# Performance work log

Hardware: AMD Instinct MI355X
Metric: run time of the kernel (lower is better)

Reference implementation:

```python
import jax, jax.numpy as jnp
import numpy as np

B, T, CIN, F, K, U, FF, N, LS = 16, 384, 64, 64, 32, 128, 1024, 64, 15
EPS = 1e-3  # keras BatchNormalization epsilon

def _conv1d(x, w):
    # x:[B,T,C], w:[K,C,F], 'same' padding, no bias
    return jax.lax.conv_general_dilated(x, w, (1,), 'SAME', dimension_numbers=('NWC', 'WIO', 'NWC'))

def _bn(x, g, b, m, v):
    # inference-mode batchnorm
    return g * (x - m) * jax.lax.rsqrt(v + EPS) + b

def _gru_seq(x, k, rk, b):
    # keras GRU (reset_after=True), gate order [z, r, h]; x:[B,T,D] -> [B,T,U]
    u = rk.shape[0]
    xp = x @ k + b[0]                      # precompute input projections [B,T,3U]
    def step(h, xt):
        rec = h @ rk + b[1]
        xz, xr, xh = jnp.split(xt, 3, axis=-1)
        rz, rr_, rh = jnp.split(rec, 3, axis=-1)
        z = jax.nn.sigmoid(xz + rz)
        r = jax.nn.sigmoid(xr + rr_)
        hh = jnp.tanh(xh + r * rh)
        hn = z * h + (1.0 - z) * hh
        return hn, hn
    h0 = jnp.zeros((x.shape[0], u), x.dtype)
    _, ys = jax.lax.scan(step, h0, jnp.swapaxes(xp, 0, 1))
    return jnp.swapaxes(ys, 0, 1)

def _cgru(xr, xi, kr, rkr, br, ki, rki, bi):
    # ComplexGRUCell: real_gru applied to both parts, imag_gru applied to both parts
    rr = _gru_seq(xr, kr, rkr, br)
    ri = _gru_seq(xi, kr, rkr, br)
    ir = _gru_seq(xr, ki, rki, bi)
    ii = _gru_seq(xi, ki, rki, bi)
    return rr - ii, ri + ir

def _forward(h_real, h_imag, conv_wr, conv_wi, bn_gr, bn_br, bn_mr, bn_vr, bn_gi, bn_bi, bn_mi, bn_vi, g0_kr, g0_rkr, g0_br, g0_ki, g0_rki, g0_bi, gs_kr, gs_rkr, gs_br, gs_ki, gs_rki, gs_bi, ff1_w, ff1_b, ff2_w, ff2_b, qr_w, qr_b, qi_w, qi_b, rr_w, rr_b, ri_w, ri_b):
    xr = _bn(_conv1d(h_real, conv_wr) - _conv1d(h_imag, conv_wi), bn_gr, bn_br, bn_mr, bn_vr)
    xi = _bn(_conv1d(h_imag, conv_wr) + _conv1d(h_real, conv_wi), bn_gi, bn_bi, bn_mi, bn_vi)
    xr, xi = _cgru(xr, xi, g0_kr, g0_rkr, g0_br, g0_ki, g0_rki, g0_bi)
    for i in range(LS):  # fixed small layer count
        xr, xi = _cgru(xr, xi, gs_kr[i], gs_rkr[i], gs_br[i], gs_ki[i], gs_rki[i], gs_bi[i])
    def ff(a):
        return jax.nn.relu(a @ ff1_w + ff1_b) @ ff2_w + ff2_b
    xr = xr + ff(xr)   # dropout is identity at inference
    xi = xi + ff(xi)
    mr = jnp.mean(xr, axis=1)
    mi = jnp.mean(xi, axis=1)
    Qr = (mr @ qr_w + qr_b) - (mi @ qi_w + qi_b)
    Qi = (mi @ qr_w + qr_b) + (mr @ qi_w + qi_b)
    Rr = (mr @ rr_w + rr_b) - (mi @ ri_w + ri_b)
    Ri = (mi @ rr_w + rr_b) + (mr @ ri_w + ri_b)
    Qr = Qr.reshape(-1, N, N); Qi = Qi.reshape(-1, N, N)
    Rr = Rr.reshape(-1, N, N); Ri = Ri.reshape(-1, N, N)
    # trace(Q Q^H) = sum |Q|^2 (real, nonnegative)
    nrm = jnp.sqrt(jnp.sum(Qr * Qr + Qi * Qi, axis=(1, 2)))[:, None, None]
    scale = jnp.sqrt(jnp.float32(N)) / nrm
    return Qr * scale, Qi * scale, Rr, Ri

def setup_inputs():
    key = jax.random.key(0)
    ks = jax.random.split(key, 20)
    s = 0.05
    def nrm(k, shape, scale=s):
        return jax.random.normal(k, shape, jnp.float32) * scale
    inp = {}
    inp['h_real'] = nrm(ks[0], (B, T, CIN), 1.0)
    inp['h_imag'] = nrm(ks[1], (B, T, CIN), 1.0)
    inp['conv_wr'] = nrm(ks[2], (K, CIN, F))
    inp['conv_wi'] = nrm(ks[3], (K, CIN, F))
    for nm in ('bn_gr', 'bn_gi', 'bn_vr', 'bn_vi'):
        inp[nm] = jnp.ones((F,), jnp.float32)
    for nm in ('bn_br', 'bn_bi', 'bn_mr', 'bn_mi'):
        inp[nm] = jnp.zeros((F,), jnp.float32)
    inp['g0_kr'] = nrm(ks[4], (F, 3 * U));  inp['g0_rkr'] = nrm(ks[5], (U, 3 * U));  inp['g0_br'] = jnp.zeros((2, 3 * U), jnp.float32)
    inp['g0_ki'] = nrm(ks[6], (F, 3 * U));  inp['g0_rki'] = nrm(ks[7], (U, 3 * U));  inp['g0_bi'] = jnp.zeros((2, 3 * U), jnp.float32)
    inp['gs_kr'] = nrm(ks[8], (LS, U, 3 * U));  inp['gs_rkr'] = nrm(ks[9], (LS, U, 3 * U));  inp['gs_br'] = jnp.zeros((LS, 2, 3 * U), jnp.float32)
    inp['gs_ki'] = nrm(ks[10], (LS, U, 3 * U)); inp['gs_rki'] = nrm(ks[11], (LS, U, 3 * U)); inp['gs_bi'] = jnp.zeros((LS, 2, 3 * U), jnp.float32)
    inp['ff1_w'] = nrm(ks[12], (U, FF)); inp['ff1_b'] = jnp.zeros((FF,), jnp.float32)
    inp['ff2_w'] = nrm(ks[13], (FF, U)); inp['ff2_b'] = jnp.zeros((U,), jnp.float32)
    inp['qr_w'] = nrm(ks[14], (U, N * N)); inp['qr_b'] = jnp.zeros((N * N,), jnp.float32)
    inp['qi_w'] = nrm(ks[15], (U, N * N)); inp['qi_b'] = jnp.zeros((N * N,), jnp.float32)
    inp['rr_w'] = nrm(ks[16], (U, N * N)); inp['rr_b'] = jnp.zeros((N * N,), jnp.float32)
    inp['ri_w'] = nrm(ks[17], (U, N * N)); inp['ri_b'] = jnp.zeros((N * N,), jnp.float32)
    return inp

def reference(h_real, h_imag, conv_wr, conv_wi, bn_gr, bn_br, bn_mr, bn_vr, bn_gi, bn_bi, bn_mi, bn_vi, g0_kr, g0_rkr, g0_br, g0_ki, g0_rki, g0_bi, gs_kr, gs_rkr, gs_br, gs_ki, gs_rki, gs_bi, ff1_w, ff1_b, ff2_w, ff2_b, qr_w, qr_b, qi_w, qi_b, rr_w, rr_b, ri_w, ri_b):
    return _forward(h_real, h_imag, conv_wr, conv_wi, bn_gr, bn_br, bn_mr, bn_vr, bn_gi, bn_bi, bn_mi, bn_vi, g0_kr, g0_rkr, g0_br, g0_ki, g0_rki, g0_bi, gs_kr, gs_rkr, gs_br, gs_ki, gs_rki, gs_bi, ff1_w, ff1_b, ff2_w, ff2_b, qr_w, qr_b, qi_w, qi_b, rr_w, rr_b, ri_w, ri_b)
```

## Files before the change

kernel.cpp:

```cpp
#include <hip/hip_runtime.h>
#include <hip/hip_bf16.h>
#include <math.h>

typedef __attribute__((ext_vector_type(8))) short short8;
typedef __attribute__((ext_vector_type(4))) float f32x4;
typedef unsigned short u16;
typedef unsigned int u32;

#define CL 16
#define NCHUNK 24
#define RING 4
#define CHSZ (16*CL*128)

__device__ __forceinline__ u16 f2bf(float f){
  u32 x = __float_as_uint(f);
  u32 r = x + 0x7fffu + ((x >> 16) & 1u);
  return (u16)(r >> 16);
}
__device__ __forceinline__ float bf2f(u16 u){
  return __uint_as_float(((u32)u) << 16);
}
__device__ __forceinline__ f32x4 mfma16(short8 a, short8 b, f32x4 c){
  return __builtin_amdgcn_mfma_f32_16x16x32_bf16(a, b, c, 0, 0, 0);
}

__global__ __launch_bounds__(256) void k_pro(
    float* S, float* ssq, u32* Flg, float* Mx, float* Macc,
    const float* __restrict__ wr, const float* __restrict__ wi,
    const float* __restrict__ w1,
    u16* WtR, u16* WtI, u16* WtIN, u16* W1t,
    const float* __restrict__ g0_kr, const float* __restrict__ g0_ki,
    const float* __restrict__ gs_kr, const float* __restrict__ gs_ki,
    const float* __restrict__ g0_rkr, const float* __restrict__ g0_rki,
    const float* __restrict__ gs_rkr, const float* __restrict__ gs_rki,
    u16* __restrict__ KT, u16* __restrict__ RKT){
  __shared__ float tile[128][33];
  int bid = blockIdx.x, tid = threadIdx.x;
  if (bid < 177){
    int i = bid*256 + tid;
    if (i < 32768){ S[i] = 0.f; return; }
    i -= 32768;
    if (i < 16){ ssq[i] = 0.f; return; }
    i -= 16;
    if (i < 4096){ Flg[i] = 0u; return; }
    i -= 4096;
    if (i < 4096){ Mx[i] = 0.f; return; }
    i -= 4096;
    if (i < 4096){ Macc[i] = 0.f; return; }
    return;
  }
  if (bid < 1201){
    int i = (bid - 177)*256 + tid;
    if (i < 131072){
      int k = i >> 12, r = i & 4095, f = r >> 6, c = r & 63;
      float a = wr[(k<<12) + (c<<6) + f];
      float b = wi[(k<<12) + (c<<6) + f];
      WtR[i] = f2bf(a); WtI[i] = f2bf(b); WtIN[i] = f2bf(-b);
    } else {
      int j = i - 131072;
      int col = j >> 7, k = j & 127;
      W1t[j] = f2bf(w1[(k<<10) + col]);
    }
    return;
  }
  {
    int bid2 = bid - 1201;
    int ct = bid2 % 12; int lm = (bid2/12) & 31; int which = bid2 / (12*32);
    int m = lm & 1, l = lm >> 1;
    int c0 = ct*32;
    for (int idx = tid; idx < 128*32; idx += 256){
      int k = idx >> 5, cc = idx & 31;
      float v;
      if (!which){
        if (l == 0) v = (k < 64) ? (m ? g0_ki : g0_kr)[k*384 + c0+cc] : 0.f;
        else        v = (m ? gs_ki : gs_kr)[((size_t)(l-1)*128 + k)*384 + c0+cc];
      } else {
        if (l == 0) v = (m ? g0_rki : g0_rkr)[k*384 + c0+cc];
        else        v = (m ? gs_rki : gs_rkr)[((size_t)(l-1)*128 + k)*384 + c0+cc];
      }
      tile[k][cc] = v;
    }
    __syncthreads();
    u16* dst = (which ? RKT : KT) + (size_t)lm*384*128;
    for (int idx = tid; idx < 32*128; idx += 256){
      int cc = idx >> 7, k = idx & 127;
      dst[(size_t)(c0+cc)*128 + k] = f2bf(tile[k][cc]);
    }
  }
}

__global__ __launch_bounds__(256) void k_conv(
    const float* __restrict__ hr, const float* __restrict__ hi,
    const u16* __restrict__ WtR, const u16* __restrict__ WtI, const u16* __restrict__ WtIN,
    const float* __restrict__ gr, const float* __restrict__ gi,
    const float* __restrict__ vr, const float* __restrict__ vi,
    const float* __restrict__ br, const float* __restrict__ bi,
    const float* __restrict__ mr, const float* __restrict__ mi,
    u16* __restrict__ X0){
  __shared__ u16 xst[2*64*64];
  int tid = threadIdx.x;
  int bid = blockIdx.x;
  int b = bid / 12, t0 = (bid % 12) * 32;
  for (int el = tid; el < 2*63*64; el += 256){
    int part = el / (63*64); int rem = el % (63*64); int row = rem >> 6; int c = rem & 63;
    int tg = t0 + row - 15;
    const float* src = part ? hi : hr;
    float v = (tg >= 0 && tg < 384) ? src[((size_t)b*384 + tg)*64 + c] : 0.f;
    int idx = (part*64 + row)*64 + c;
    int byte = (idx<<1) ^ ((row&7)<<4);
    *(u16*)((char*)xst + byte) = f2bf(v);
  }
  __syncthreads();
  int lane = tid & 63, wid = tid >> 6, lr = lane & 15, lg = lane >> 4;
  f32x4 accr = {0,0,0,0}, acci = {0,0,0,0};
  f32x4 accr2 = {0,0,0,0}, acci2 = {0,0,0,0};
  for (int k = 0; k < 32; ++k){
    int row = lr + k;
    int row2 = row + 16;
    int swz = (row&7)<<4, swz2 = (row2&7)<<4;
    for (int ch = 0; ch < 2; ++ch){
      int c0 = ch*32 + lg*8;
      int idxr  = (0*64 + row )*64 + c0;
      int idxi  = (1*64 + row )*64 + c0;
      int idxr2 = (0*64 + row2)*64 + c0;
      int idxi2 = (1*64 + row2)*64 + c0;
      short8 ar  = *(const short8*)((const char*)xst + ((idxr <<1) ^ swz));
      short8 ai  = *(const short8*)((const char*)xst + ((idxi <<1) ^ swz));
      short8 ar2 = *(const short8*)((const char*)xst + ((idxr2<<1) ^ swz2));
      short8 ai2 = *(const short8*)((const char*)xst + ((idxi2<<1) ^ swz2));
      size_t wb = ((size_t)(k*64 + wid*16 + lr))*64 + c0;
      short8 bwr = *(const short8*)(WtR + wb);
      short8 bwi = *(const short8*)(WtI + wb);
      short8 bwn = *(const short8*)(WtIN + wb);
      accr  = mfma16(ar,  bwr, accr);
      accr  = mfma16(ai,  bwn, accr);
      acci  = mfma16(ai,  bwr, acci);
      acci  = mfma16(ar,  bwi, acci);
      accr2 = mfma16(ar2, bwr, accr2);
      accr2 = mfma16(ai2, bwn, accr2);
      acci2 = mfma16(ai2, bwr, acci2);
      acci2 = mfma16(ar2, bwi, acci2);
    }
  }
  int f = wid*16 + lr;
  float sr_ = gr[f] * rsqrtf(vr[f] + 1e-3f), or_ = br[f] - mr[f]*sr_;
  float si_ = gi[f] * rsqrtf(vi[f] + 1e-3f), oi_ = bi[f] - mi[f]*si_;
  for (int r = 0; r < 4; ++r){
    int t  = t0 + lg*4 + r;
    int t2 = t0 + 16 + lg*4 + r;
    X0[(((size_t)0*16 + b)*384 + t )*64 + f] = f2bf(accr[r] *sr_ + or_);
    X0[(((size_t)1*16 + b)*384 + t )*64 + f] = f2bf(acci[r] *si_ + oi_);
    X0[(((size_t)0*16 + b)*384 + t2)*64 + f] = f2bf(accr2[r]*sr_ + or_);
    X0[(((size_t)1*16 + b)*384 + t2)*64 + f] = f2bf(acci2[r]*si_ + oi_);
  }
}

__global__ __launch_bounds__(512,1) void k_scanp(
    const u16* __restrict__ X0, const u16* __restrict__ KT, const u16* __restrict__ RKT,
    const float* __restrict__ g0_br, const float* __restrict__ g0_bi,
    const float* __restrict__ gs_br, const float* __restrict__ gs_bi,
    u16* __restrict__ HC, u16* __restrict__ HS15, u32* Flg)
{
  int bid = blockIdx.x;
  int l = bid >> 2, s = bid & 3;

  __shared__ u16 xs[16*CL*128];
  __shared__ u16 hs2[2*16*128];
  __shared__ float bsh[4][128];

  int tid = threadIdx.x, lane = tid & 63, wv = tid >> 6, lr = lane & 15, lg = lane >> 4;
  int m = s >> 1;

  const float* Bsrc = (l == 0) ? (m ? g0_bi : g0_br)
                               : ((m ? gs_bi : gs_br) + (size_t)(l-1)*768);
  if (tid < 128){
    int j = tid;
    bsh[0][j] = Bsrc[j]       + Bsrc[384 + j];
    bsh[1][j] = Bsrc[128 + j] + Bsrc[384 + 128 + j];
    bsh[2][j] = Bsrc[256 + j];
    bsh[3][j] = Bsrc[384 + 256 + j];
  }
  for (int i = tid; i < 2048; i += 512) ((u32*)hs2)[i] = 0u;

  const u16* Kp  = KT  + (size_t)(l*2 + m)*384*128;
  const u16* RKp = RKT + (size_t)(l*2 + m)*384*128;
  int cz = wv*16 + lr;
  short8 wz[8], wr2[8], whx[4], whr[4];
  #pragma unroll
  for (int ks = 0; ks < 4; ++ks){
    wz[ks]    = *(const short8*)(RKp + (size_t)cz*128 + ks*32 + lg*8);
    wz[4+ks]  = *(const short8*)(Kp  + (size_t)cz*128 + ks*32 + lg*8);
    wr2[ks]   = *(const short8*)(RKp + (size_t)(128+cz)*128 + ks*32 + lg*8);
    wr2[4+ks] = *(const short8*)(Kp  + (size_t)(128+cz)*128 + ks*32 + lg*8);
    whx[ks]   = *(const short8*)(Kp  + (size_t)(256+cz)*128 + ks*32 + lg*8);
    whr[ks]   = *(const short8*)(RKp + (size_t)(256+cz)*128 + ks*32 + lg*8);
  }

  float hreg[4] = {0.f, 0.f, 0.f, 0.f};

  __syncthreads();
  float bz, br_, bhx, bhr;
  {
    int j = wv*16 + lr;
    bz = bsh[0][j]; br_ = bsh[1][j]; bhx = bsh[2][j]; bhr = bsh[3][j];
  }

  u32* prodF = Flg;
  u32* consF = Flg + 2048;
  int sA = (s & 1) ? 1 : 0, sB = (s & 1) ? 2 : 3;
  int pA = (l-1)*4 + sA, pB = (l-1)*4 + sB;
  float sgn = (s & 1) ? 1.f : -1.f;
  int p = s & 1;
  int me = l*4 + s;

  for (int c = 0; c < NCHUNK; ++c){
    int t0 = c * CL;
    int slot = c & (RING-1);

    if (tid == 0){
      int guard = 0;
      if (l > 0){
        while (__hip_atomic_load(&prodF[pA*32], __ATOMIC_RELAXED, __HIP_MEMORY_SCOPE_AGENT) < (u32)(c+1) ||
               __hip_atomic_load(&prodF[pB*32], __ATOMIC_RELAXED, __HIP_MEMORY_SCOPE_AGENT) < (u32)(c+1)){
          __builtin_amdgcn_s_sleep(1);
          if (++guard > 10000000) break;
        }
      }
      if (l < 15 && c >= RING){
        guard = 0;
        while (__hip_atomic_load(&consF[me*32], __ATOMIC_RELAXED, __HIP_MEMORY_SCOPE_AGENT) < (u32)(2*(c-RING+1))){
          __builtin_amdgcn_s_sleep(1);
          if (++guard > 10000000) break;
        }
      }
    }
    __syncthreads();

    if (l == 0){
      short8 v[8];
      #pragma unroll
      for (int it = 0; it < 8; ++it){
        int g = tid + it*512;
        int k8 = g & 15, ttv = (g>>4) & 15, b = g >> 8;
        short8 t = {0,0,0,0,0,0,0,0};
        if (k8 < 8) t = *(const short8*)(X0 + (((size_t)p*16 + b)*384 + t0 + ttv)*64 + k8*8);
        v[it] = t;
      }
      asm volatile("" ::: "memory");
      #pragma unroll
      for (int it = 0; it < 8; ++it){
        int g = tid + it*512;
        int k8 = g & 15, ttv = (g>>4) & 15, b = g >> 8;
        int byte = (((b*CL + ttv)*128 + k8*8) << 1) ^ ((b&7)<<4);
        *(short8*)((char*)xs + byte) = v[it];
      }
      __syncthreads();
    } else {
      __builtin_amdgcn_fence(__ATOMIC_ACQUIRE, "agent");
      const u16* baseA = HC + ((size_t)pA*RING + slot)*CHSZ;
      const u16* baseB = HC + ((size_t)pB*RING + slot)*CHSZ;
      short8 va[8], vb[8];
      #pragma unroll
      for (int it = 0; it < 8; ++it){
        int g = tid + it*512;
        int k8 = g & 15, ttv = (g>>4) & 15, b = g >> 8;
        size_t si = ((size_t)b*CL + ttv)*128 + k8*8;
        va[it] = *(const short8*)(baseA + si);
        vb[it] = *(const short8*)(baseB + si);
      }
      asm volatile("" ::: "memory");
      #pragma unroll
      for (int it = 0; it < 8; ++it){
        int g = tid + it*512;
        int k8 = g & 15, ttv = (g>>4) & 15, b = g >> 8;
        short8 o;
        #pragma unroll
        for (int e = 0; e < 8; ++e){
          float f = bf2f((u16)va[it][e]) + sgn*bf2f((u16)vb[it][e]);
          o[e] = (short)f2bf(f);
        }
        int byte = (((b*CL + ttv)*128 + k8*8) << 1) ^ ((b&7)<<4);
        *(short8*)((char*)xs + byte) = o;
      }
      __syncthreads();
      if (tid == 0){
        __hip_atomic_fetch_add(&consF[pA*32], 1u, __ATOMIC_RELAXED, __HIP_MEMORY_SCOPE_AGENT);
        __hip_atomic_fetch_add(&consF[pB*32], 1u, __ATOMIC_RELAXED, __HIP_MEMORY_SCOPE_AGENT);
      }
    }

    u16* outp;
    int Tp, tbase;
    if (l < 15){
      outp = HC + ((size_t)me*RING + slot)*CHSZ;
      Tp = CL; tbase = 0;
    } else {
      outp = HS15 + (size_t)s*16*384*128;
      Tp = 384; tbase = t0;
    }

    for (int q = 0; q < 4; ++q){
      f32x4 xpz[4], xpr[4], xph[4];
      #pragma unroll
      for (int t2 = 0; t2 < 4; ++t2){
        int tt = q*4 + t2;
        short8 ax[4];
        #pragma unroll
        for (int ks = 0; ks < 4; ++ks){
          int xb = (((lr*CL + tt)*128 + ks*32 + lg*8) << 1) ^ ((lr&7)<<4);
          ax[ks] = *(const short8*)((char*)xs + xb);
        }
        f32x4 az  = {bz, bz, bz, bz};
        f32x4 ar  = {br_, br_, br_, br_};
        f32x4 ahx = {bhx, bhx, bhx, bhx};
        #pragma unroll
        for (int ks = 0; ks < 4; ++ks){
          az  = mfma16(ax[ks], wz[4+ks],  az);
          ar  = mfma16(ax[ks], wr2[4+ks], ar);
          ahx = mfma16(ax[ks], whx[ks],   ahx);
        }
        xpz[t2] = az; xpr[t2] = ar; xph[t2] = ahx;
      }
      #pragma unroll
      for (int t2 = 0; t2 < 4; ++t2){
        int tt = q*4 + t2;
        int hp = tt & 1;
        short8 ah[4];
        #pragma unroll
        for (int ks = 0; ks < 4; ++ks){
          int hb = hp*4096 + (((lr*128 + ks*32 + lg*8) << 1) ^ ((lr&7)<<4));
          ah[ks] = *(const short8*)((char*)hs2 + hb);
        }
        f32x4 az  = xpz[t2];
        f32x4 ar  = xpr[t2];
        f32x4 ahr = {bhr, bhr, bhr, bhr};
        #pragma unroll
        for (int ks = 0; ks < 4; ++ks){
          az  = mfma16(ah[ks], wz[ks],  az);
          ar  = mfma16(ah[ks], wr2[ks], ar);
          ahr = mfma16(ah[ks], whr[ks], ahr);
        }
        int j = wv*16 + lr;
        #pragma unroll
        for (int r = 0; r < 4; ++r){
          int b = lg*4 + r;
          float z  = 1.f/(1.f + __expf(-az[r]));
          float rg = 1.f/(1.f + __expf(-ar[r]));
          float pre = xph[t2][r] + rg*ahr[r];
          pre = fminf(fmaxf(pre, -15.f), 15.f);
          float e2 = __expf(2.f*pre);
          float hh = (e2 - 1.f)/(e2 + 1.f);
          float hn = z*hreg[r] + (1.f - z)*hh;
          hreg[r] = hn;
          u16 hb16 = f2bf(hn);
          int byte = ((hp^1)*4096) + ((((b*128 + j) << 1)) ^ ((b&7)<<4));
          *(u16*)((char*)hs2 + byte) = hb16;
          outp[((size_t)b*Tp + tbase + tt)*128 + j] = hb16;
        }
        __syncthreads();
      }
    }

    if (l < 15 && tid == 0){
      __hip_atomic_fetch_add(&prodF[me*32], 1u, __ATOMIC_RELEASE, __HIP_MEMORY_SCOPE_AGENT);
    }
  }
}

__global__ __launch_bounds__(256) void k_ffs(const u16* __restrict__ HS, const u16* __restrict__ W1t,
                                             const float* __restrict__ b1, float* __restrict__ S,
                                             float* __restrict__ Mx){
  int bid = blockIdx.x;
  int part = bid / 384; int rem = bid % 384;
  int b = rem / 24; int rem2 = rem % 24;
  int t0 = (rem2 / 4) * 64, c0 = (rem2 % 4) * 256;
  int tid = threadIdx.x, lane = tid & 63, wid = tid >> 6, lr = lane & 15, lg = lane >> 4;
  int sA = part ? 1 : 0, sB = part ? 2 : 3;
  float sgn = part ? 1.f : -1.f;
  short8 af[4][4];
  #pragma unroll
  for (int rt = 0; rt < 4; ++rt)
    #pragma unroll
    for (int ks = 0; ks < 4; ++ks){
      size_t i1 = (((size_t)sA*16 + b)*384 + t0 + rt*16 + lr)*128 + ks*32 + lg*8;
      size_t i2 = (((size_t)sB*16 + b)*384 + t0 + rt*16 + lr)*128 + ks*32 + lg*8;
      short8 va = *(const short8*)(HS + i1);
      short8 vb = *(const short8*)(HS + i2);
      short8 o;
      #pragma unroll
      for (int e = 0; e < 8; ++e){
        float f = bf2f((u16)va[e]) + sgn*bf2f((u16)vb[e]);
        o[e] = (short)f2bf(f);
      }
      af[rt][ks] = o;
    }
  if (rem2 % 4 == 0 && wid == 0){
    #pragma unroll
    for (int ks = 0; ks < 4; ++ks){
      #pragma unroll
      for (int e = 0; e < 8; ++e){
        float s = 0.f;
        #pragma unroll
        for (int rt = 0; rt < 4; ++rt) s += bf2f((u16)af[rt][ks][e]);
        s += __shfl_xor(s, 1, 64);
        s += __shfl_xor(s, 2, 64);
        s += __shfl_xor(s, 4, 64);
        s += __shfl_xor(s, 8, 64);
        if (lr == 0) atomicAdd(&Mx[((size_t)part*16 + b)*128 + ks*32 + lg*8 + e], s);
      }
    }
  }
  for (int ctl = 0; ctl < 4; ++ctl){
    int col = c0 + wid*64 + ctl*16 + lr;
    short8 bf[4];
    #pragma unroll
    for (int ks = 0; ks < 4; ++ks)
      bf[ks] = *(const short8*)(W1t + (size_t)col*128 + ks*32 + lg*8);
    float bias = b1[col];
    float ssum = 0.f;
    #pragma unroll
    for (int rt = 0; rt < 4; ++rt){
      f32x4 acc = {0,0,0,0};
      #pragma unroll
      for (int ks = 0; ks < 4; ++ks) acc = mfma16(af[rt][ks], bf[ks], acc);
      #pragma unroll
      for (int r = 0; r < 4; ++r) ssum += fmaxf(acc[r] + bias, 0.f);
    }
    ssum += __shfl_xor(ssum, 16, 64);
    ssum += __shfl_xor(ssum, 32, 64);
    if (lg == 0) atomicAdd(&S[((size_t)part*16 + b)*1024 + col], ssum);
  }
}

__global__ void k_combp(const float* __restrict__ S, const float* __restrict__ w2,
                        float* __restrict__ Macc){
  int bid = blockIdx.x; int u = threadIdx.x;
  int pb = bid >> 2, fq = bid & 3;
  const float* Sp = S + (size_t)pb*1024;
  float acc = 0.f;
  for (int f = fq*256; f < fq*256 + 256; ++f) acc += Sp[f] * w2[(size_t)f*128 + u];
  atomicAdd(&Macc[pb*128 + u], acc);
}

__global__ __launch_bounds__(256) void k_qr(const float* __restrict__ Mx,
    const float* __restrict__ Macc, const float* __restrict__ b2,
    const float* __restrict__ qr_w, const float* __restrict__ qr_b,
    const float* __restrict__ qi_w, const float* __restrict__ qi_b,
    const float* __restrict__ rr_w, const float* __restrict__ rr_b,
    const float* __restrict__ ri_w, const float* __restrict__ ri_b,
    float* __restrict__ out, float* __restrict__ ssq){
  __shared__ float smr[128], smi[128];
  int bid = blockIdx.x; int tid = threadIdx.x;
  int b = bid >> 4; int o = (bid & 15)*256 + tid;
  if (tid < 128){
    smr[tid] = (Mx[b*128 + tid]        + Macc[b*128 + tid]       ) * (1.f/384.f) + b2[tid];
    smi[tid] = (Mx[(16 + b)*128 + tid] + Macc[(16 + b)*128 + tid]) * (1.f/384.f) + b2[tid];
  }
  __syncthreads();
  float aq=0, bq=0, cq=0, dq=0, ar=0, br2=0, cr=0, dr=0;
  for (int u = 0; u < 128; ++u){
    float mr = smr[u], mi = smi[u];
    float wqr = qr_w[(size_t)u*4096 + o], wqi = qi_w[(size_t)u*4096 + o];
    float wrr = rr_w[(size_t)u*4096 + o], wri = ri_w[(size_t)u*4096 + o];
    aq += mr*wqr;  bq += mi*wqi;  cq += mi*wqr;  dq += mr*wqi;
    ar += mr*wrr;  br2 += mi*wri; cr += mi*wrr;  dr += mr*wri;
  }
  float Qr = (aq + qr_b[o]) - (bq + qi_b[o]);
  float Qi = (cq + qr_b[o]) + (dq + qi_b[o]);
  float Rr = (ar + rr_b[o]) - (br2 + ri_b[o]);
  float Ri = (cr + rr_b[o]) + (dr + ri_b[o]);
  out[(size_t)b*4096 + o] = Qr;
  out[65536 + (size_t)b*4096 + o] = Qi;
  out[131072 + (size_t)b*4096 + o] = Rr;
  out[196608 + (size_t)b*4096 + o] = Ri;
  float ss = Qr*Qr + Qi*Qi;
  for (int off = 32; off; off >>= 1) ss += __shfl_down(ss, off, 64);
  if ((tid & 63) == 0) atomicAdd(&ssq[b], ss);
}

__global__ void k_scale(float* __restrict__ out, const float* __restrict__ ssq){
  int i = blockIdx.x*256 + threadIdx.x;
  int b = (i >> 12) & 15;
  float s = 8.f / sqrtf(ssq[b]);
  out[i] *= s;
}

extern "C" void kernel_launch(void* const* d_in, const int* in_sizes, int n_in,
                              void* d_out, int out_size, void* d_ws, size_t ws_size,
                              hipStream_t stream){
  const float* h_real = (const float*)d_in[0];
  const float* h_imag = (const float*)d_in[1];
  const float* conv_wr = (const float*)d_in[2];
  const float* conv_wi = (const float*)d_in[3];
  const float* bn_gr = (const float*)d_in[4];
  const float* bn_gi = (const float*)d_in[5];
  const float* bn_vr = (const float*)d_in[6];
  const float* bn_vi = (const float*)d_in[7];
  const float* bn_br = (const float*)d_in[8];
  const float* bn_bi = (const float*)d_in[9];
  const float* bn_mr = (const float*)d_in[10];
  const float* bn_mi = (const float*)d_in[11];
  const float* g0_kr = (const float*)d_in[12];
  const float* g0_rkr = (const float*)d_in[13];
  const float* g0_br = (const float*)d_in[14];
  const float* g0_ki = (const float*)d_in[15];
  const float* g0_rki = (const float*)d_in[16];
  const float* g0_bi = (const float*)d_in[17];
  const float* gs_kr = (const float*)d_in[18];
  const float* gs_rkr = (const float*)d_in[19];
  const float* gs_br = (const float*)d_in[20];
  const float* gs_ki = (const float*)d_in[21];
  const float* gs_rki = (const float*)d_in[22];
  const float* gs_bi = (const float*)d_in[23];
  const float* ff1_w = (const float*)d_in[24];
  const float* ff1_b = (const float*)d_in[25];
  const float* ff2_w = (const float*)d_in[26];
  const float* ff2_b = (const float*)d_in[27];
  const float* qr_w = (const float*)d_in[28];
  const float* qr_b = (const float*)d_in[29];
  const float* qi_w = (const float*)d_in[30];
  const float* qi_b = (const float*)d_in[31];
  const float* rr_w = (const float*)d_in[32];
  const float* rr_b = (const float*)d_in[33];
  const float* ri_w = (const float*)d_in[34];
  const float* ri_b = (const float*)d_in[35];

  char* ws = (char*)d_ws; size_t off = 0;
  auto carve = [&](size_t bytes)->char*{ char* p = ws + off; off += (bytes + 255) & ~(size_t)255; return p; };
  u16* X0   = (u16*)carve((size_t)2*16*384*64*2);
  u16* HC   = (u16*)carve((size_t)64*RING*CHSZ*2);
  u16* HS15 = (u16*)carve((size_t)4*16*384*128*2);
  u16* KT   = (u16*)carve((size_t)16*2*384*128*2);
  u16* RKT  = (u16*)carve((size_t)16*2*384*128*2);
  u16* WtR  = (u16*)carve(131072*2);
  u16* WtI  = (u16*)carve(131072*2);
  u16* WtIN = (u16*)carve(131072*2);
  u16* W1t  = (u16*)carve(131072*2);
  u32* Flg  = (u32*)carve(4096*4);
  float* S  = (float*)carve(32768*4);
  float* Mx = (float*)carve(4096*4);
  float* Macc = (float*)carve(4096*4);
  float* ssq = (float*)carve(256);

  k_pro<<<1969, 256, 0, stream>>>(S, ssq, Flg, Mx, Macc,
                                  conv_wr, conv_wi, ff1_w, WtR, WtI, WtIN, W1t,
                                  g0_kr, g0_ki, gs_kr, gs_ki,
                                  g0_rkr, g0_rki, gs_rkr, gs_rki, KT, RKT);
  k_conv<<<192, 256, 0, stream>>>(h_real, h_imag, WtR, WtI, WtIN,
                                  bn_gr, bn_gi, bn_vr, bn_vi, bn_br, bn_bi, bn_mr, bn_mi, X0);
  k_scanp<<<64, 512, 0, stream>>>(X0, KT, RKT, g0_br, g0_bi, gs_br, gs_bi,
                                  HC, HS15, Flg);
  k_ffs<<<768, 256, 0, stream>>>(HS15, W1t, ff1_b, S, Mx);
  k_combp<<<128, 128, 0, stream>>>(S, ff2_w, Macc);
  k_qr<<<256, 256, 0, stream>>>(Mx, Macc, ff2_b, qr_w, qr_b, qi_w, qi_b,
                                rr_w, rr_b, ri_w, ri_b, (float*)d_out, ssq);
  k_scale<<<512, 256, 0, stream>>>((float*)d_out, ssq);
}
```

Before: 1.063 ms.

## Fuse conv into scan kernel with per-window flags so layer 0 starts early

Folds the conv+batchnorm kernel into the persistent scan kernel as 192 extra blocks. Each conv block signals a per-time-window flag, and layer-0 scan blocks spin on those flags per chunk instead of waiting for a separate kernel launch to finish. This removes one launch boundary and overlaps conv work with the start of the recurrent scan. The costs are spin-waiting, larger shared memory per block, and the assumption that the 64 scan blocks and the conv blocks can be co-resident or scheduled so they do not deadlock.

Result: no change. 1.061 ms (-0.3%).

```diff
diff --git a/kernel.cpp b/kernel.cpp
--- a/kernel.cpp
+++ b/kernel.cpp
@@ -36,21 +36,21 @@
     u16* __restrict__ KT, u16* __restrict__ RKT){
   __shared__ float tile[128][33];
   int bid = blockIdx.x, tid = threadIdx.x;
-  if (bid < 177){
+  if (bid < 179){
     int i = bid*256 + tid;
     if (i < 32768){ S[i] = 0.f; return; }
     i -= 32768;
     if (i < 16){ ssq[i] = 0.f; return; }
     i -= 16;
-    if (i < 4096){ Flg[i] = 0u; return; }
-    i -= 4096;
+    if (i < 4608){ Flg[i] = 0u; return; }
+    i -= 4608;
     if (i < 4096){ Mx[i] = 0.f; return; }
     i -= 4096;
     if (i < 4096){ Macc[i] = 0.f; return; }
     return;
   }
-  if (bid < 1201){
-    int i = (bid - 177)*256 + tid;
+  if (bid < 1203){
+    int i = (bid - 179)*256 + tid;
     if (i < 131072){
       int k = i >> 12, r = i & 4095, f = r >> 6, c = r & 63;
       float a = wr[(k<<12) + (c<<6) + f];
@@ -64,7 +64,7 @@
     return;
   }
   {
-    int bid2 = bid - 1201;
+    int bid2 = bid - 1203;
     int ct = bid2 % 12; int lm = (bid2/12) & 31; int which = bid2 / (12*32);
     int m = lm & 1, l = lm >> 1;
     int c0 = ct*32;
@@ -89,86 +89,94 @@
   }
 }
 
-__global__ __launch_bounds__(256) void k_conv(
+__global__ __launch_bounds__(512,1) void k_scanp(
+    u16* __restrict__ X0, const u16* __restrict__ KT, const u16* __restrict__ RKT,
+    const float* __restrict__ g0_br, const float* __restrict__ g0_bi,
+    const float* __restrict__ gs_br, const float* __restrict__ gs_bi,
+    u16* __restrict__ HC, u16* __restrict__ HS15, u32* Flg,
     const float* __restrict__ hr, const float* __restrict__ hi,
     const u16* __restrict__ WtR, const u16* __restrict__ WtI, const u16* __restrict__ WtIN,
     const float* __restrict__ gr, const float* __restrict__ gi,
     const float* __restrict__ vr, const float* __restrict__ vi,
     const float* __restrict__ br, const float* __restrict__ bi,
-    const float* __restrict__ mr, const float* __restrict__ mi,
-    u16* __restrict__ X0){
-  __shared__ u16 xst[2*64*64];
-  int tid = threadIdx.x;
+    const float* __restrict__ mr, const float* __restrict__ mi)
+{
+  __shared__ __align__(16) char smem[75776];
   int bid = blockIdx.x;
-  int b = bid / 12, t0 = (bid % 12) * 32;
-  for (int el = tid; el < 2*63*64; el += 256){
-    int part = el / (63*64); int rem = el % (63*64); int row = rem >> 6; int c = rem & 63;
-    int tg = t0 + row - 15;
-    const float* src = part ? hi : hr;
-    float v = (tg >= 0 && tg < 384) ? src[((size_t)b*384 + tg)*64 + c] : 0.f;
-    int idx = (part*64 + row)*64 + c;
-    int byte = (idx<<1) ^ ((row&7)<<4);
-    *(u16*)((char*)xst + byte) = f2bf(v);
-  }
-  __syncthreads();
-  int lane = tid & 63, wid = tid >> 6, lr = lane & 15, lg = lane >> 4;
-  f32x4 accr = {0,0,0,0}, acci = {0,0,0,0};
-  f32x4 accr2 = {0,0,0,0}, acci2 = {0,0,0,0};
-  for (int k = 0; k < 32; ++k){
-    int row = lr + k;
-    int row2 = row + 16;
-    int swz = (row&7)<<4, swz2 = (row2&7)<<4;
-    for (int ch = 0; ch < 2; ++ch){
-      int c0 = ch*32 + lg*8;
-      int idxr  = (0*64 + row )*64 + c0;
-      int idxi  = (1*64 + row )*64 + c0;
-      int idxr2 = (0*64 + row2)*64 + c0;
-      int idxi2 = (1*64 + row2)*64 + c0;
-      short8 ar  = *(const short8*)((const char*)xst + ((idxr <<1) ^ swz));
-      short8 ai  = *(const short8*)((const char*)xst + ((idxi <<1) ^ swz));
-      short8 ar2 = *(const short8*)((const char*)xst + ((idxr2<<1) ^ swz2));
-      short8 ai2 = *(const short8*)((const char*)xst + ((idxi2<<1) ^ swz2));
-      size_t wb = ((size_t)(k*64 + wid*16 + lr))*64 + c0;
-      short8 bwr = *(const short8*)(WtR + wb);
-      short8 bwi = *(const short8*)(WtI + wb);
-      short8 bwn = *(const short8*)(WtIN + wb);
-      accr  = mfma16(ar,  bwr, accr);
-      accr  = mfma16(ai,  bwn, accr);
-      acci  = mfma16(ai,  bwr, acci);
-      acci  = mfma16(ar,  bwi, acci);
-      accr2 = mfma16(ar2, bwr, accr2);
-      accr2 = mfma16(ai2, bwn, accr2);
-      acci2 = mfma16(ai2, bwr, acci2);
-      acci2 = mfma16(ar2, bwi, acci2);
-    }
-  }
-  int f = wid*16 + lr;
-  float sr_ = gr[f] * rsqrtf(vr[f] + 1e-3f), or_ = br[f] - mr[f]*sr_;
-  float si_ = gi[f] * rsqrtf(vi[f] + 1e-3f), oi_ = bi[f] - mi[f]*si_;
-  for (int r = 0; r < 4; ++r){
-    int t  = t0 + lg*4 + r;
-    int t2 = t0 + 16 + lg*4 + r;
-    X0[(((size_t)0*16 + b)*384 + t )*64 + f] = f2bf(accr[r] *sr_ + or_);
-    X0[(((size_t)1*16 + b)*384 + t )*64 + f] = f2bf(acci[r] *si_ + oi_);
-    X0[(((size_t)0*16 + b)*384 + t2)*64 + f] = f2bf(accr2[r]*sr_ + or_);
-    X0[(((size_t)1*16 + b)*384 + t2)*64 + f] = f2bf(acci2[r]*si_ + oi_);
-  }
-}
-
-__global__ __launch_bounds__(512,1) void k_scanp(
-    const u16* __restrict__ X0, const u16* __restrict__ KT, const u16* __restrict__ RKT,
-    const float* __restrict__ g0_br, const float* __restrict__ g0_bi,
-    const float* __restrict__ gs_br, const float* __restrict__ gs_bi,
-    u16* __restrict__ HC, u16* __restrict__ HS15, u32* Flg)
-{
-  int bid = blockIdx.x;
+  int tid = threadIdx.x, lane = tid & 63, wv = tid >> 6, lr = lane & 15, lg = lane >> 4;
+  u32* convF = Flg + 4096;
+
+  if (bid >= 64){
+    u16* xst = (u16*)smem;
+    int cb = bid - 64;
+    int w = cb >> 4, b = cb & 15;
+    int t0 = w * 32;
+    for (int el = tid; el < 2*63*64; el += 512){
+      int part = el / (63*64); int rem = el % (63*64); int row = rem >> 6; int c = rem & 63;
+      int tg = t0 + row - 15;
+      const float* src = part ? hi : hr;
+      float v = (tg >= 0 && tg < 384) ? src[((size_t)b*384 + tg)*64 + c] : 0.f;
+      int idx = (part*64 + row)*64 + c;
+      int byte = (idx<<1) ^ ((row&7)<<4);
+      *(u16*)((char*)xst + byte) = f2bf(v);
+    }
+    __syncthreads();
+    if (wv < 4){
+      int wid = wv;
+      f32x4 accr = {0,0,0,0}, acci = {0,0,0,0};
+      f32x4 accr2 = {0,0,0,0}, acci2 = {0,0,0,0};
+      for (int k = 0; k < 32; ++k){
+        int row = lr + k;
+        int row2 = row + 16;
+        int swz = (row&7)<<4, swz2 = (row2&7)<<4;
+        for (int ch = 0; ch < 2; ++ch){
+          int c0 = ch*32 + lg*8;
+          int idxr  = (0*64 + row )*64 + c0;
+          int idxi  = (1*64 + row )*64 + c0;
+          int idxr2 = (0*64 + row2)*64 + c0;
+          int idxi2 = (1*64 + row2)*64 + c0;
+          short8 ar  = *(const short8*)((const char*)xst + ((idxr <<1) ^ swz));
+          short8 ai  = *(const short8*)((const char*)xst + ((idxi <<1) ^ swz));
+          short8 ar2 = *(const short8*)((const char*)xst + ((idxr2<<1) ^ swz2));
+          short8 ai2 = *(const short8*)((const char*)xst + ((idxi2<<1) ^ swz2));
+          size_t wb = ((size_t)(k*64 + wid*16 + lr))*64 + c0;
+          short8 bwr = *(const short8*)(WtR + wb);
+          short8 bwi = *(const short8*)(WtI + wb);
+          short8 bwn = *(const short8*)(WtIN + wb);
+          accr  = mfma16(ar,  bwr, accr);
+          accr  = mfma16(ai,  bwn, accr);
+          acci  = mfma16(ai,  bwr, acci);
+          acci  = mfma16(ar,  bwi, acci);
+          accr2 = mfma16(ar2, bwr, accr2);
+          accr2 = mfma16(ai2, bwn, accr2);
+          acci2 = mfma16(ai2, bwr, acci2);
+          acci2 = mfma16(ar2, bwi, acci2);
+        }
+      }
+      int f = wid*16 + lr;
+      float sr_ = gr[f] * rsqrtf(vr[f] + 1e-3f), or_ = br[f] - mr[f]*sr_;
+      float si_ = gi[f] * rsqrtf(vi[f] + 1e-3f), oi_ = bi[f] - mi[f]*si_;
+      for (int r = 0; r < 4; ++r){
+        int t  = t0 + lg*4 + r;
+        int t2 = t0 + 16 + lg*4 + r;
+        X0[(((size_t)0*16 + b)*384 + t )*64 + f] = f2bf(accr[r] *sr_ + or_);
+        X0[(((size_t)1*16 + b)*384 + t )*64 + f] = f2bf(acci[r] *si_ + oi_);
+        X0[(((size_t)0*16 + b)*384 + t2)*64 + f] = f2bf(accr2[r]*sr_ + or_);
+        X0[(((size_t)1*16 + b)*384 + t2)*64 + f] = f2bf(acci2[r]*si_ + oi_);
+      }
+    }
+    __syncthreads();
+    if (tid == 0){
+      __hip_atomic_fetch_add(&convF[w*32], 1u, __ATOMIC_RELEASE, __HIP_MEMORY_SCOPE_AGENT);
+    }
+    return;
+  }
+
   int l = bid >> 2, s = bid & 3;
-
-  __shared__ u16 xs[16*CL*128];
-  __shared__ u16 hs2[2*16*128];
-  __shared__ float bsh[4][128];
-
-  int tid = threadIdx.x, lane = tid & 63, wv = tid >> 6, lr = lane & 15, lg = lane >> 4;
+  u16* xs  = (u16*)smem;
+  u16* hs2 = (u16*)(smem + 65536);
+  float (*bsh)[128] = (float(*)[128])(smem + 65536 + 8192);
+
   int m = s >> 1;
 
   const float* Bsrc = (l == 0) ? (m ? g0_bi : g0_br)
@@ -225,6 +233,11 @@
           __builtin_amdgcn_s_sleep(1);
           if (++guard > 10000000) break;
         }
+      } else {
+        while (__hip_atomic_load(&convF[(c>>1)*32], __ATOMIC_RELAXED, __HIP_MEMORY_SCOPE_AGENT) < 16u){
+          __builtin_amdgcn_s_sleep(1);
+          if (++guard > 10000000) break;
+        }
       }
       if (l < 15 && c >= RING){
         guard = 0;
@@ -237,6 +250,7 @@
     __syncthreads();
 
     if (l == 0){
+      __builtin_amdgcn_fence(__ATOMIC_ACQUIRE, "agent");
       short8 v[8];
       #pragma unroll
       for (int it = 0; it < 8; ++it){
@@ -536,20 +550,20 @@
   u16* WtI  = (u16*)carve(131072*2);
   u16* WtIN = (u16*)carve(131072*2);
   u16* W1t  = (u16*)carve(131072*2);
-  u32* Flg  = (u32*)carve(4096*4);
+  u32* Flg  = (u32*)carve(4608*4);
   float* S  = (float*)carve(32768*4);
   float* Mx = (float*)carve(4096*4);
   float* Macc = (float*)carve(4096*4);
   float* ssq = (float*)carve(256);
 
-  k_pro<<<1969, 256, 0, stream>>>(S, ssq, Flg, Mx, Macc,
+  k_pro<<<1971, 256, 0, stream>>>(S, ssq, Flg, Mx, Macc,
                                   conv_wr, conv_wi, ff1_w, WtR, WtI, WtIN, W1t,
                                   g0_kr, g0_ki, gs_kr, gs_ki,
                                   g0_rkr, g0_rki, gs_rkr, gs_rki, KT, RKT);
-  k_conv<<<192, 256, 0, stream>>>(h_real, h_imag, WtR, WtI, WtIN,
-                                  bn_gr, bn_gi, bn_vr, bn_vi, bn_br, bn_bi, bn_mr, bn_mi, X0);
-  k_scanp<<<64, 512, 0, stream>>>(X0, KT, RKT, g0_br, g0_bi, gs_br, gs_bi,
-                                  HC, HS15, Flg);
+  k_scanp<<<256, 512, 0, stream>>>(X0, KT, RKT, g0_br, g0_bi, gs_br, gs_bi,
+                                   HC, HS15, Flg,
+                                   h_real, h_imag, WtR, WtI, WtIN,
+                                   bn_gr, bn_gi, bn_vr, bn_vi, bn_br, bn_bi, bn_mr, bn_mi);
   k_ffs<<<768, 256, 0, stream>>>(HS15, W1t, ff1_b, S, Mx);
   k_combp<<<128, 128, 0, stream>>>(S, ff2_w, Macc);
   k_qr<<<256, 256, 0, stream>>>(Mx, Macc, ff2_b, qr_w, qr_b, qi_w, qi_b,
```
